# Kernel tuning notes

Measured on AMD Instinct MI355X. Metric: run time of the kernel, lower is better.

The kernel has to match this reference:

```python
import jax, jax.numpy as jnp
import numpy as np

HEADS = 6
PS = 7  # window size
DN = ('NCHW', 'OIHW', 'NCHW')


def _conv1x1(x, w):
    return jax.lax.conv_general_dilated(x, w, (1, 1), 'VALID', dimension_numbers=DN)


def _dwconv3(x, w, groups):
    return jax.lax.conv_general_dilated(x, w, (1, 1), 'SAME', dimension_numbers=DN,
                                        feature_group_count=groups)


def _l2norm(t, eps=1e-12):
    # matches torch F.normalize(dim=-1): x / max(||x||_2, eps)
    n = jnp.sqrt(jnp.sum(t * t, axis=-1, keepdims=True))
    return t / jnp.maximum(n, eps)


def setup_inputs() -> dict:
    key = jax.random.key(0)
    k1, k2, k3, k4 = jax.random.split(key, 4)
    B, C, H, W = 2, 180, 448, 448
    x = jax.random.normal(k1, (B, C, H, W), dtype=jnp.float32)
    temperature = jnp.ones((HEADS, 1, 1), dtype=jnp.float32)
    w_qkv = jax.random.normal(k2, (3 * C, C, 1, 1), dtype=jnp.float32) * 0.05
    w_dw = jax.random.normal(k3, (3 * C, 1, 3, 3), dtype=jnp.float32) * 0.05
    w_proj = jax.random.normal(k4, (C, C, 1, 1), dtype=jnp.float32) * 0.05
    return {'x': x, 'temperature': temperature, 'w_qkv': w_qkv, 'w_dw': w_dw, 'w_proj': w_proj}


def reference(x, temperature, w_qkv, w_dw, w_proj):
    b, c, H, W = x.shape
    d = c // HEADS
    hh, ww = H // PS, W // PS

    qkv = _dwconv3(_conv1x1(x, w_qkv), w_dw, 3 * c)  # [b, 3c, H, W]
    q, k, v = jnp.split(qkv, 3, axis=1)

    def rearr(t):
        # 'b (head d) (h ph) (w pw) -> b (h w) head d (ph pw)'
        t = t.reshape(b, HEADS, d, hh, PS, ww, PS)
        t = t.transpose(0, 3, 5, 1, 2, 4, 6)  # b, hh, ww, head, d, ph, pw
        return t.reshape(b, hh * ww, HEADS, d, PS * PS)

    q, k, v = rearr(q), rearr(k), rearr(v)
    q = _l2norm(q)
    k = _l2norm(k)

    # channel-channel attention per window: [b, n_win, head, d, d]
    attn = jnp.einsum('bnhdp,bnhep->bnhde', q, k) * temperature
    attn = jax.nn.softmax(attn, axis=-1)
    out = jnp.einsum('bnhde,bnhep->bnhdp', attn, v)

    # inverse rearrange: 'b (h w) head d (ph pw) -> b (head d) (h ph) (w pw)'
    out = out.reshape(b, hh, ww, HEADS, d, PS, PS)
    out = out.transpose(0, 3, 4, 1, 5, 2, 6).reshape(b, c, H, W)
    return _conv1x1(out, w_proj)
```

## Files before the change

### kernel.cpp

```cpp
#include <hip/hip_runtime.h>

#define HW 200704
#define WIMG 448
#define VPLANE 229376

typedef __attribute__((ext_vector_type(4))) unsigned int u32x4;
typedef __attribute__((ext_vector_type(4))) float f32x4;
typedef __attribute__((ext_vector_type(8))) short s16x8;

static __device__ __forceinline__ unsigned short f2bf(float f) {
    union { float f; unsigned int u; } v; v.f = f;
    unsigned int u = v.u;
    unsigned int r = u + 0x7FFFu + ((u >> 16) & 1u);
    return (unsigned short)(r >> 16);
}
static __device__ __forceinline__ float bf2f(unsigned short s) {
    union { unsigned int u; float f; } v; v.u = ((unsigned int)s) << 16;
    return v.f;
}

__global__ __launch_bounds__(256) void wconv_kernel(
    const float* __restrict__ src, unsigned short* __restrict__ dst,
    int ocu, int octot)
{
    int idx = blockIdx.x * 256 + threadIdx.x;
    if (idx >= octot * 24) return;
    int row = idx / 24, ch = idx - row * 24;
    unsigned short u[8];
#pragma unroll
    for (int e = 0; e < 8; ++e) {
        int k = ch * 8 + e;
        u[e] = (row < ocu && k < 180) ? f2bf(src[row * 180 + k]) : (unsigned short)0;
    }
    *(u32x4*)(dst + row * 192 + ch * 8) = *(const u32x4*)u;
}

__global__ __launch_bounds__(256) void transpose_cast_kernel(
    const float* __restrict__ x, unsigned short* __restrict__ xT)
{
    const int p0 = blockIdx.x * 64;
    const int tid = threadIdx.x;
    const int pl = tid & 63;

    __shared__ float T[180 * 65];

    for (int ic = tid >> 6; ic < 180; ic += 4)
        T[ic * 65 + pl] = x[(size_t)ic * HW + p0 + pl];
    __syncthreads();

    const int cg = tid >> 6;
    unsigned short* drow = xT + ((size_t)p0 + pl) * 192;
#pragma unroll
    for (int i = 0; i < 6; ++i) {
        int k0 = (cg * 6 + i) * 8;
        unsigned short u[8];
#pragma unroll
        for (int e = 0; e < 8; ++e)
            u[e] = (k0 + e < 180) ? f2bf(T[(k0 + e) * 65 + pl]) : (unsigned short)0;
        *(u32x4*)(drow + k0) = *(const u32x4*)u;
    }
}

__global__ __launch_bounds__(256) void gemm_qkv_kernel(
    const unsigned short* __restrict__ xT, const unsigned short* __restrict__ wqb,
    unsigned short* __restrict__ A)
{
    const int d    = blockIdx.x;
    const int orig = (d & 7) * 882 + (d >> 3);
    const int pt   = orig / 9;
    const int ocb  = (orig - pt * 9) * 64;
    const int pix0 = pt * 256;
    const int tid  = threadIdx.x;
    const int l    = tid & 63;
    const int q    = tid >> 6;
    const int r15  = l & 15;
    const int g4   = l >> 4;

    __shared__ __align__(16) unsigned short xs[2][256 * 64];

    auto stage = [&](int c, int buf) {
#pragma unroll
        for (int i = 0; i < 8; ++i) {
            int slot = i * 256 + tid;
            int px   = slot >> 3;
            int g    = slot & 7;
            const unsigned short* src =
                xT + ((size_t)pix0 + px) * 192 + c * 64 + ((g ^ (px & 7)) << 3);
            __builtin_amdgcn_global_load_lds(
                (const __attribute__((address_space(1))) unsigned int*)(const void*)src,
                (__attribute__((address_space(3))) unsigned int*)(void*)(&xs[buf][slot * 8]),
                16, 0, 0);
        }
    };

    f32x4 acc[4][4];
#pragma unroll
    for (int nt = 0; nt < 4; ++nt)
#pragma unroll
        for (int mi = 0; mi < 4; ++mi) acc[nt][mi] = (f32x4){0.f, 0.f, 0.f, 0.f};

    const unsigned short* wrow = wqb + (size_t)(ocb + r15) * 192;

    stage(0, 0);
    __syncthreads();

    for (int c = 0; c < 3; ++c) {
        if (c < 2) stage(c + 1, (c + 1) & 1);
        const unsigned short* xb = xs[c & 1];
#pragma unroll
        for (int kk = 0; kk < 2; ++kk) {
            s16x8 aX[4], bW[4];
#pragma unroll
            for (int nt = 0; nt < 4; ++nt) {
                int px = q * 64 + nt * 16 + r15;
                aX[nt] = __builtin_bit_cast(s16x8, *(const u32x4*)(
                    xb + px * 64 + (((kk * 4 + g4) ^ (px & 7)) << 3)));
            }
#pragma unroll
            for (int mi = 0; mi < 4; ++mi)
                bW[mi] = __builtin_bit_cast(s16x8, *(const u32x4*)(
                    wrow + mi * 16 * 192 + c * 64 + kk * 32 + g4 * 8));
#pragma unroll
            for (int nt = 0; nt < 4; ++nt)
#pragma unroll
                for (int mi = 0; mi < 4; ++mi)
                    acc[nt][mi] = __builtin_amdgcn_mfma_f32_16x16x32_bf16(
                        aX[nt], bW[mi], acc[nt][mi], 0, 0, 0);
        }
        if (c < 2) __syncthreads();
    }

#pragma unroll
    for (int mi = 0; mi < 4; ++mi) {
        int oc = ocb + mi * 16 + r15;
        if (oc < 540) {
            unsigned short* orow = A + (size_t)oc * HW + pix0 + q * 64 + g4 * 4;
#pragma unroll
            for (int nt = 0; nt < 4; ++nt) {
                uint2 v;
                v.x = (unsigned int)f2bf(acc[nt][mi][0]) |
                      ((unsigned int)f2bf(acc[nt][mi][1]) << 16);
                v.y = (unsigned int)f2bf(acc[nt][mi][2]) |
                      ((unsigned int)f2bf(acc[nt][mi][3]) << 16);
                *(uint2*)(orow + nt * 16) = v;
            }
        }
    }
}

__global__ __launch_bounds__(256) void dw_kernel(
    const unsigned short* __restrict__ A, const float* __restrict__ wdw,
    unsigned short* __restrict__ Bw)
{
    const int wrow = blockIdx.x;
    const int c    = blockIdx.y;
    const int tid  = threadIdx.x;

    const int part = c / 180;
    const int rem  = c - part * 180;
    const int head = rem / 30;
    const int dc   = rem - head * 30;

    __shared__ __align__(8) float Ls[9 * 454];

    float w9[9];
#pragma unroll
    for (int i = 0; i < 9; ++i) w9[i] = wdw[c * 9 + i];

    const int y0 = wrow * 7;
    const unsigned int* Ac32 = (const unsigned int*)(A + (size_t)c * HW);
    for (int idx = tid; idx < 2016; idx += 256) {
        int r  = idx / 224;
        int c2 = idx - r * 224;
        int y  = y0 + r - 1;
        unsigned int v = ((unsigned)y < 448u) ? Ac32[y * 224 + c2] : 0u;
        float2 f2;
        f2.x = bf2f((unsigned short)(v & 0xffffu));
        f2.y = bf2f((unsigned short)(v >> 16));
        *(float2*)(Ls + r * 454 + 2 + 2 * c2) = f2;
    }
    if (tid < 18) {
        int r = tid >> 1;
        Ls[r * 454 + ((tid & 1) ? 450 : 1)] = 0.f;
    }
    __syncthreads();

    unsigned short* dstb = Bw +
        ((size_t)(head * 3 + part) * 30 + dc) * VPLANE + (size_t)wrow * 3584;

    for (int idx = tid; idx < 448; idx += 256) {
        int wo = idx / 7;
        int pp = idx - wo * 7;
        dstb[wo * 56 + 49 + pp] = 0;
    }

#pragma unroll
    for (int it = 0; it < 2; ++it) {
        int x = it * 256 + tid;
        if (x < 448) {
            int wo = x / 7;
            int pw = x - wo * 7;
            unsigned short* op = dstb + wo * 56 + pw;

            const float* Lb = Ls + x + 1;
            float a0 = Lb[0], a1 = Lb[1], a2 = Lb[2];
            Lb += 454;
            float b0 = Lb[0], b1 = Lb[1], b2 = Lb[2];
#pragma unroll
            for (int ph = 0; ph < 7; ++ph) {
                Lb += 454;
                float c0 = Lb[0], c1 = Lb[1], c2v = Lb[2];
                float acc = w9[0]*a0 + w9[1]*a1 + w9[2]*a2
                          + w9[3]*b0 + w9[4]*b1 + w9[5]*b2
                          + w9[6]*c0 + w9[7]*c1 + w9[8]*c2v;
                op[ph * 7] = f2bf(acc);
                a0 = b0; a1 = b1; a2 = b2;
                b0 = c0; b1 = c1; b2 = c2v;
            }
        }
    }
}

__global__ __launch_bounds__(256) void attn2_kernel(
    const unsigned short* __restrict__ Bw,
    const float* __restrict__ temperature,
    unsigned short* __restrict__ Cwt)
{
    __shared__ __align__(16) unsigned short lds[4][6144];
    __shared__ float invs[4][64];

    const int w    = threadIdx.x >> 6;
    const int l    = threadIdx.x & 63;
    const int wg   = blockIdx.x;
    const int head = blockIdx.y;
    const int win  = wg * 4 + w;
    const float temp = temperature[head];
    unsigned short* U = lds[w];
    float* inv = invs[w];
    const int r15 = l & 15;
    const int g4  = l >> 4;

    {
        const unsigned short* plane0 =
            Bw + (size_t)(head * 3) * 30 * VPLANE + (size_t)win * 56;
#pragma unroll
        for (int i = 0; i < 8; ++i) {
            int part = i >> 2;
            int row  = ((i & 3) << 3) | (l >> 3);
            int c    = l & 7;
            u32x4 v = {0u, 0u, 0u, 0u};
            if (row < 30 && c < 7)
                v = *(const u32x4*)(plane0 + (size_t)(part * 30 + row) * VPLANE + c * 8);
            *(u32x4*)(U + part * 2048 + row * 64 + ((c ^ (row & 7)) << 3)) = v;
        }
    }
    {
        const unsigned short* vplane =
            Bw + (size_t)(head * 3 + 2) * 30 * VPLANE + (size_t)win * 56;
        for (int j = 0; j < 23; ++j) {
            int idx = j * 64 + l;
            if (idx < 1470) {
                int dc = idx / 49;
                int p  = idx - dc * 49;
                unsigned short val = vplane[(size_t)dc * VPLANE + p];
                int col = (((dc >> 3) ^ (p & 3)) << 3) | (dc & 7);
                U[4096 + p * 32 + col] = val;
            }
        }
        int c30 = ((3 ^ (l & 3)) << 3) | 6;
        U[4096 + l * 32 + c30]     = 0;
        U[4096 + l * 32 + c30 + 1] = 0;
    }
    __syncthreads();

    s16x8 aQ[2][2], bK[2][2];
#pragma unroll
    for (int mi = 0; mi < 2; ++mi)
#pragma unroll
        for (int kk = 0; kk < 2; ++kk) {
            int r  = mi * 16 + r15;
            int gk = kk * 4 + g4;
            int so = ((gk ^ (r & 7)) << 3);
            aQ[mi][kk] = __builtin_bit_cast(s16x8, *(const u32x4*)(U + r * 64 + so));
            bK[mi][kk] = __builtin_bit_cast(s16x8, *(const u32x4*)(U + 2048 + r * 64 + so));
        }

    f32x4 s[2][2], dq[2], dk[2];
#pragma unroll
    for (int mi = 0; mi < 2; ++mi) {
        dq[mi] = (f32x4){0.f, 0.f, 0.f, 0.f};
        dk[mi] = (f32x4){0.f, 0.f, 0.f, 0.f};
#pragma unroll
        for (int nj = 0; nj < 2; ++nj) s[mi][nj] = (f32x4){0.f, 0.f, 0.f, 0.f};
    }

#pragma unroll
    for (int kk = 0; kk < 2; ++kk) {
#pragma unroll
        for (int mi = 0; mi < 2; ++mi) {
#pragma unroll
            for (int nj = 0; nj < 2; ++nj)
                s[mi][nj] = __builtin_amdgcn_mfma_f32_16x16x32_bf16(
                    aQ[mi][kk], bK[nj][kk], s[mi][nj], 0, 0, 0);
            dq[mi] = __builtin_amdgcn_mfma_f32_16x16x32_bf16(
                aQ[mi][kk], aQ[mi][kk], dq[mi], 0, 0, 0);
            dk[mi] = __builtin_amdgcn_mfma_f32_16x16x32_bf16(
                bK[mi][kk], bK[mi][kk], dk[mi], 0, 0, 0);
        }
    }

#pragma unroll
    for (int mi = 0; mi < 2; ++mi)
#pragma unroll
        for (int reg = 0; reg < 4; ++reg) {
            int row = g4 * 4 + reg;
            if (row == r15) {
                inv[mi * 16 + row]      = 1.f / fmaxf(sqrtf(dq[mi][reg]), 1e-12f);
                inv[32 + mi * 16 + row] = 1.f / fmaxf(sqrtf(dk[mi][reg]), 1e-12f);
            }
        }
    __syncthreads();

    float pr[2][2][4];
    float cinvk0 = inv[32 + r15];
    float cinvk1 = inv[32 + 16 + r15];
#pragma unroll
    for (int mi = 0; mi < 2; ++mi)
#pragma unroll
        for (int reg = 0; reg < 4; ++reg) {
            float qi = inv[mi * 16 + g4 * 4 + reg];
            float v0 = s[mi][0][reg] * qi * cinvk0 * temp;
            float v1 = s[mi][1][reg] * qi * cinvk1 * temp;
            if (16 + r15 >= 30) v1 = -1e30f;
            float m = fmaxf(v0, v1);
#pragma unroll
            for (int off = 1; off < 16; off <<= 1) m = fmaxf(m, __shfl_xor(m, off));
            float e0 = __expf(v0 - m);
            float e1 = __expf(v1 - m);
            float sum = e0 + e1;
#pragma unroll
            for (int off = 1; off < 16; off <<= 1) sum += __shfl_xor(sum, off);
            float rs = 1.f / sum;
            pr[mi][0][reg] = e0 * rs;
            pr[mi][1][reg] = e1 * rs;
        }

#pragma unroll
    for (int mi = 0; mi < 2; ++mi)
#pragma unroll
        for (int nj = 0; nj < 2; ++nj)
#pragma unroll
            for (int reg = 0; reg < 4; ++reg) {
                int row = mi * 16 + g4 * 4 + reg;
                int col = nj * 16 + r15;
                int scol = (((col >> 3) ^ (row & 3)) << 3) | (col & 7);
                U[row * 32 + scol] = f2bf(pr[mi][nj][reg]);
            }
    __syncthreads();

    s16x8 aP[2], bV[4];
#pragma unroll
    for (int mi = 0; mi < 2; ++mi) {
        int i = mi * 16 + r15;
        aP[mi] = __builtin_bit_cast(s16x8,
                 *(const u32x4*)(U + i * 32 + ((g4 ^ (i & 3)) << 3)));
    }
#pragma unroll
    for (int nt = 0; nt < 4; ++nt) {
        int p = nt * 16 + r15;
        bV[nt] = __builtin_bit_cast(s16x8,
                 *(const u32x4*)(U + 4096 + p * 32 + ((g4 ^ (p & 3)) << 3)));
    }
    f32x4 o[2][4];
#pragma unroll
    for (int mi = 0; mi < 2; ++mi)
#pragma unroll
        for (int nt = 0; nt < 4; ++nt) {
            o[mi][nt] = (f32x4){0.f, 0.f, 0.f, 0.f};
            o[mi][nt] = __builtin_amdgcn_mfma_f32_16x16x32_bf16(
                aP[mi], bV[nt], o[mi][nt], 0, 0, 0);
        }

    unsigned short* dst = Cwt + ((size_t)win * 49) * 192 + head * 30;
#pragma unroll
    for (int mi = 0; mi < 2; ++mi) {
        int ch0 = mi * 16 + g4 * 4;
#pragma unroll
        for (int nt = 0; nt < 4; ++nt) {
            int p = nt * 16 + r15;
            if (p < 49) {
                unsigned int lo = (unsigned int)f2bf(o[mi][nt][0]) |
                                  ((unsigned int)f2bf(o[mi][nt][1]) << 16);
                *(unsigned int*)(dst + (size_t)p * 192 + ch0) = lo;
                if (ch0 + 2 < 30) {
                    unsigned int hi = (unsigned int)f2bf(o[mi][nt][2]) |
                                      ((unsigned int)f2bf(o[mi][nt][3]) << 16);
                    *(unsigned int*)(dst + (size_t)p * 192 + ch0 + 2) = hi;
                }
            }
        }
    }
    if (head == 5 && g4 == 0) {
        unsigned short* zrow = Cwt + ((size_t)win * 49) * 192 + 180;
#pragma unroll
        for (int nt = 0; nt < 4; ++nt) {
            int p = nt * 16 + r15;
            if (p < 49) {
                *(unsigned int*)(zrow + (size_t)p * 192 + 0) = 0u;
                *(unsigned int*)(zrow + (size_t)p * 192 + 2) = 0u;
                *(unsigned int*)(zrow + (size_t)p * 192 + 4) = 0u;
            }
        }
    }
}

__global__ __launch_bounds__(256) void gemm_proj_kernel(
    const unsigned short* __restrict__ Cwt, const unsigned short* __restrict__ wpb,
    float* __restrict__ out)
{
    const int d    = blockIdx.x;
    const int orig = (d & 7) * 294 + (d >> 3);
    const int pt   = orig / 3;
    const int ocb  = (orig - pt * 3) * 64;
    const int pix0 = pt * 256;
    const int tid  = threadIdx.x;
    const int l    = tid & 63;
    const int q    = tid >> 6;
    const int r15  = l & 15;
    const int g4   = l >> 4;

    __shared__ __align__(16) unsigned short xs[2][256 * 64];

    auto stage = [&](int c, int buf) {
#pragma unroll
        for (int i = 0; i < 8; ++i) {
            int slot = i * 256 + tid;
            int px   = slot >> 3;
            int g    = slot & 7;
            const unsigned short* src =
                Cwt + ((size_t)pix0 + px) * 192 + c * 64 + ((g ^ (px & 7)) << 3);
            __builtin_amdgcn_global_load_lds(
                (const __attribute__((address_space(1))) unsigned int*)(const void*)src,
                (__attribute__((address_space(3))) unsigned int*)(void*)(&xs[buf][slot * 8]),
                16, 0, 0);
        }
    };

    f32x4 acc[4][4];
#pragma unroll
    for (int mi = 0; mi < 4; ++mi)
#pragma unroll
        for (int nt = 0; nt < 4; ++nt) acc[mi][nt] = (f32x4){0.f, 0.f, 0.f, 0.f};

    const unsigned short* wrow = wpb + (size_t)(ocb + r15) * 192;

    stage(0, 0);
    __syncthreads();

    for (int c = 0; c < 3; ++c) {
        if (c < 2) stage(c + 1, (c + 1) & 1);
        const unsigned short* xb = xs[c & 1];
#pragma unroll
        for (int kk = 0; kk < 2; ++kk) {
            s16x8 aW[4], bX[4];
#pragma unroll
            for (int mi = 0; mi < 4; ++mi)
                aW[mi] = __builtin_bit_cast(s16x8, *(const u32x4*)(
                    wrow + mi * 16 * 192 + c * 64 + kk * 32 + g4 * 8));
#pragma unroll
            for (int nt = 0; nt < 4; ++nt) {
                int px = q * 64 + nt * 16 + r15;
                bX[nt] = __builtin_bit_cast(s16x8, *(const u32x4*)(
                    xb + px * 64 + (((kk * 4 + g4) ^ (px & 7)) << 3)));
            }
#pragma unroll
            for (int mi = 0; mi < 4; ++mi)
#pragma unroll
                for (int nt = 0; nt < 4; ++nt)
                    acc[mi][nt] = __builtin_amdgcn_mfma_f32_16x16x32_bf16(
                        aW[mi], bX[nt], acc[mi][nt], 0, 0, 0);
        }
        if (c < 2) __syncthreads();
    }

    int poff[4];
#pragma unroll
    for (int nt = 0; nt < 4; ++nt) {
        int P = pix0 + q * 64 + nt * 16 + r15;
        int win = P / 49, p = P - win * 49;
        int ph = p / 7, pw2 = p - ph * 7;
        poff[nt] = ((win >> 6) * 7 + ph) * WIMG + (win & 63) * 7 + pw2;
    }
#pragma unroll
    for (int mi = 0; mi < 4; ++mi) {
#pragma unroll
        for (int reg = 0; reg < 4; ++reg) {
            int oc = ocb + mi * 16 + g4 * 4 + reg;
            if (oc < 180) {
#pragma unroll
                for (int nt = 0; nt < 4; ++nt)
                    out[(size_t)oc * HW + poff[nt]] = acc[mi][nt][reg];
            }
        }
    }
}

extern "C" void kernel_launch(void* const* d_in, const int* in_sizes, int n_in,
                              void* d_out, int out_size, void* d_ws, size_t ws_size,
                              hipStream_t stream) {
    const float* x           = (const float*)d_in[0];
    const float* temperature = (const float*)d_in[1];
    const float* w_qkv       = (const float*)d_in[2];
    const float* w_dw        = (const float*)d_in[3];
    const float* w_proj      = (const float*)d_in[4];
    float* out = (float*)d_out;

    if (ws_size < 618921984ull) return;
    unsigned short* xT  = (unsigned short*)d_ws;
    unsigned short* A   = (unsigned short*)((char*)d_ws + 77070336ull);
    unsigned short* Bw  = (unsigned short*)((char*)d_ws + 293830656ull);
    unsigned short* Cwt = (unsigned short*)((char*)d_ws + 541556736ull);
    unsigned short* wqb = (unsigned short*)((char*)d_ws + 618627072ull);
    unsigned short* wpb = (unsigned short*)((char*)d_ws + 618848256ull);

    wconv_kernel<<<dim3(54), 256, 0, stream>>>(w_qkv, wqb, 540, 576);
    wconv_kernel<<<dim3(18), 256, 0, stream>>>(w_proj, wpb, 180, 192);

    for (int b = 0; b < 2; ++b) {
        const float* xb = x + (size_t)b * 180 * HW;
        float* ob = out + (size_t)b * 180 * HW;
        transpose_cast_kernel<<<dim3(HW / 64), 256, 0, stream>>>(xb, xT);
        gemm_qkv_kernel<<<dim3(7056), 256, 0, stream>>>(xT, wqb, A);
        dw_kernel<<<dim3(64, 540), 256, 0, stream>>>(A, w_dw, Bw);
        attn2_kernel<<<dim3(1024, 6), 256, 0, stream>>>(Bw, temperature, Cwt);
        gemm_proj_kernel<<<dim3(2352), 256, 0, stream>>>(Cwt, wpb, ob);
    }
}
```

Baseline: 1.341 ms.

## Single-buffer GEMM LDS staging and read depthwise conv inputs directly from global

New measurement: 1.538 ms. 14.7% more time.

```diff
diff --git a/kernel.cpp b/kernel.cpp
--- a/kernel.cpp
+++ b/kernel.cpp
@@ -76,9 +76,9 @@
     const int r15  = l & 15;
     const int g4   = l >> 4;
 
-    __shared__ __align__(16) unsigned short xs[2][256 * 64];
-
-    auto stage = [&](int c, int buf) {
+    __shared__ __align__(16) unsigned short xs[256 * 64];
+
+    auto stage = [&](int c) {
 #pragma unroll
         for (int i = 0; i < 8; ++i) {
             int slot = i * 256 + tid;
@@ -88,7 +88,7 @@
                 xT + ((size_t)pix0 + px) * 192 + c * 64 + ((g ^ (px & 7)) << 3);
             __builtin_amdgcn_global_load_lds(
                 (const __attribute__((address_space(1))) unsigned int*)(const void*)src,
-                (__attribute__((address_space(3))) unsigned int*)(void*)(&xs[buf][slot * 8]),
+                (__attribute__((address_space(3))) unsigned int*)(void*)(&xs[slot * 8]),
                 16, 0, 0);
         }
     };
@@ -101,12 +101,9 @@
 
     const unsigned short* wrow = wqb + (size_t)(ocb + r15) * 192;
 
-    stage(0, 0);
-    __syncthreads();
-
     for (int c = 0; c < 3; ++c) {
-        if (c < 2) stage(c + 1, (c + 1) & 1);
-        const unsigned short* xb = xs[c & 1];
+        stage(c);
+        __syncthreads();
 #pragma unroll
         for (int kk = 0; kk < 2; ++kk) {
             s16x8 aX[4], bW[4];
@@ -114,7 +111,7 @@
             for (int nt = 0; nt < 4; ++nt) {
                 int px = q * 64 + nt * 16 + r15;
                 aX[nt] = __builtin_bit_cast(s16x8, *(const u32x4*)(
-                    xb + px * 64 + (((kk * 4 + g4) ^ (px & 7)) << 3)));
+                    xs + px * 64 + (((kk * 4 + g4) ^ (px & 7)) << 3)));
             }
 #pragma unroll
             for (int mi = 0; mi < 4; ++mi)
@@ -161,29 +158,12 @@
     const int head = rem / 30;
     const int dc   = rem - head * 30;
 
-    __shared__ __align__(8) float Ls[9 * 454];
-
     float w9[9];
 #pragma unroll
     for (int i = 0; i < 9; ++i) w9[i] = wdw[c * 9 + i];
 
     const int y0 = wrow * 7;
-    const unsigned int* Ac32 = (const unsigned int*)(A + (size_t)c * HW);
-    for (int idx = tid; idx < 2016; idx += 256) {
-        int r  = idx / 224;
-        int c2 = idx - r * 224;
-        int y  = y0 + r - 1;
-        unsigned int v = ((unsigned)y < 448u) ? Ac32[y * 224 + c2] : 0u;
-        float2 f2;
-        f2.x = bf2f((unsigned short)(v & 0xffffu));
-        f2.y = bf2f((unsigned short)(v >> 16));
-        *(float2*)(Ls + r * 454 + 2 + 2 * c2) = f2;
-    }
-    if (tid < 18) {
-        int r = tid >> 1;
-        Ls[r * 454 + ((tid & 1) ? 450 : 1)] = 0.f;
-    }
-    __syncthreads();
+    const unsigned short* Ac = A + (size_t)c * HW;
 
     unsigned short* dstb = Bw +
         ((size_t)(head * 3 + part) * 30 + dc) * VPLANE + (size_t)wrow * 3584;
@@ -202,14 +182,21 @@
             int pw = x - wo * 7;
             unsigned short* op = dstb + wo * 56 + pw;
 
-            const float* Lb = Ls + x + 1;
-            float a0 = Lb[0], a1 = Lb[1], a2 = Lb[2];
-            Lb += 454;
-            float b0 = Lb[0], b1 = Lb[1], b2 = Lb[2];
+            auto ld3 = [&](int y, float& L, float& C, float& R) {
+                if ((unsigned)y < 448u) {
+                    const unsigned short* row = Ac + (size_t)y * WIMG;
+                    L = (x > 0)   ? bf2f(row[x - 1]) : 0.f;
+                    C = bf2f(row[x]);
+                    R = (x < 447) ? bf2f(row[x + 1]) : 0.f;
+                } else { L = C = R = 0.f; }
+            };
+
+            float a0, a1, a2, b0, b1, b2, c0, c1, c2v;
+            ld3(y0 - 1, a0, a1, a2);
+            ld3(y0,     b0, b1, b2);
 #pragma unroll
             for (int ph = 0; ph < 7; ++ph) {
-                Lb += 454;
-                float c0 = Lb[0], c1 = Lb[1], c2v = Lb[2];
+                ld3(y0 + ph + 1, c0, c1, c2v);
                 float acc = w9[0]*a0 + w9[1]*a1 + w9[2]*a2
                           + w9[3]*b0 + w9[4]*b1 + w9[5]*b2
                           + w9[6]*c0 + w9[7]*c1 + w9[8]*c2v;
@@ -429,9 +416,9 @@
     const int r15  = l & 15;
     const int g4   = l >> 4;
 
-    __shared__ __align__(16) unsigned short xs[2][256 * 64];
-
-    auto stage = [&](int c, int buf) {
+    __shared__ __align__(16) unsigned short xs[256 * 64];
+
+    auto stage = [&](int c) {
 #pragma unroll
         for (int i = 0; i < 8; ++i) {
             int slot = i * 256 + tid;
@@ -441,7 +428,7 @@
                 Cwt + ((size_t)pix0 + px) * 192 + c * 64 + ((g ^ (px & 7)) << 3);
             __builtin_amdgcn_global_load_lds(
                 (const __attribute__((address_space(1))) unsigned int*)(const void*)src,
-                (__attribute__((address_space(3))) unsigned int*)(void*)(&xs[buf][slot * 8]),
+                (__attribute__((address_space(3))) unsigned int*)(void*)(&xs[slot * 8]),
                 16, 0, 0);
         }
     };
@@ -454,12 +441,9 @@
 
     const unsigned short* wrow = wpb + (size_t)(ocb + r15) * 192;
 
-    stage(0, 0);
-    __syncthreads();
-
     for (int c = 0; c < 3; ++c) {
-        if (c < 2) stage(c + 1, (c + 1) & 1);
-        const unsigned short* xb = xs[c & 1];
+        stage(c);
+        __syncthreads();
 #pragma unroll
         for (int kk = 0; kk < 2; ++kk) {
             s16x8 aW[4], bX[4];
@@ -471,7 +455,7 @@
             for (int nt = 0; nt < 4; ++nt) {
                 int px = q * 64 + nt * 16 + r15;
                 bX[nt] = __builtin_bit_cast(s16x8, *(const u32x4*)(
-                    xb + px * 64 + (((kk * 4 + g4) ^ (px & 7)) << 3)));
+                    xs + px * 64 + (((kk * 4 + g4) ^ (px & 7)) << 3)));
             }
 #pragma unroll
             for (int mi = 0; mi < 4; ++mi)
```
